# Kernel tuning notes

Hardware: AMD Instinct MI355X
Metric: run time of the kernel (lower is better)

## Reference

```python
import jax, jax.numpy as jnp
import numpy as np
from math import sqrt

MUL = 256        # multiplicity of every irrep slot
N = 20000        # batch (edges/nodes)
FS = MUL * 1 * MUL  # flat size of each uvw weight path (u=256, v=1, w=256)

def _cg_tensors():
    # real-basis Wigner-3j (Clebsch-Gordan) tensors for l <= 1, e3nn normalization (sum of squares = 1)
    C000 = np.ones((1, 1, 1))
    eye3 = np.eye(3) / sqrt(3.0)
    C011 = eye3.reshape(1, 3, 3)
    C101 = eye3.reshape(3, 1, 3)
    C110 = eye3.reshape(3, 3, 1)
    eps = np.zeros((3, 3, 3))
    eps[0, 1, 2] = eps[1, 2, 0] = eps[2, 0, 1] = 1.0
    eps[0, 2, 1] = eps[2, 1, 0] = eps[1, 0, 2] = -1.0
    C111 = eps / sqrt(6.0)
    return C000, C011, C101, C110, C111

_C000, _C011, _C101, _C110, _C111 = [jnp.asarray(c, dtype=jnp.float32) for c in _cg_tensors()]

# normalization: alpha = sqrt((2*l_out+1) / sum_{paths with same i_out} mul1*mul2)
_A0 = sqrt(1.0 / (2 * MUL))   # l_out=0: dim 1, fan sum = 256+256 = 512
_A1 = sqrt(3.0 / (3 * MUL))   # l_out=1: dim 3, fan sum = 256*3 = 768

# (i_in1, i_in2, i_out, CG, alpha) — order defines weight layout
PATHS = [
    (0, 0, 0, _C000, _A0),
    (0, 1, 1, _C011, _A1),
    (1, 0, 1, _C101, _A1),
    (1, 1, 0, _C110, _A0),
    (1, 1, 1, _C111, _A1),
]

def setup_inputs() -> dict:
    key = jax.random.key(0)
    k1, k2, k3 = jax.random.split(key, 3)
    x1 = jax.random.normal(k1, (N, 4 * MUL), dtype=jnp.float32)   # 256x0e (256) + 256x1e (768)
    x2 = jax.random.normal(k2, (N, 4), dtype=jnp.float32)         # 1x0e (1) + 1x1e (3)
    w = jax.random.normal(k3, (5 * FS,), dtype=jnp.float32)
    # rescale=True: scale init weights by 1/sqrt(slices_fan_in[i_out]); fan_in(uvw)=mul1*mul2=256
    k0 = 1.0 / sqrt(2 * MUL)   # i_out=0: 256+256
    k1_ = 1.0 / sqrt(3 * MUL)  # i_out=1: 256*3
    scales = jnp.concatenate([jnp.full((FS,), s, dtype=jnp.float32) for s in (k0, k1_, k1_, k0, k1_)])
    weight = w * scales
    return {"x1": x1, "x2": x2, "weight": weight}

def reference(x1, x2, weight):
    n = x1.shape[0]
    x1_segs = (x1[:, :MUL].reshape(n, MUL, 1), x1[:, MUL:].reshape(n, MUL, 3))
    x2_segs = (x2[:, :1].reshape(n, 1, 1), x2[:, 1:].reshape(n, 1, 3))
    outs = [jnp.zeros((n, MUL, 1), x1.dtype), jnp.zeros((n, MUL, 3), x1.dtype)]
    off = 0
    for (ia, ib, io, cg, alpha) in PATHS:
        w = weight[off:off + FS].reshape(MUL, 1, MUL)
        off += FS
        outs[io] = outs[io] + alpha * jnp.einsum('uvw,ijk,zui,zvj->zwk', w, cg, x1_segs[ia], x2_segs[ib])
    return jnp.concatenate([outs[0].reshape(n, MUL), outs[1].reshape(n, 3 * MUL)], axis=-1)
```

## Files before the change

kernel.cpp:

```cpp
#include <hip/hip_runtime.h>


typedef short bf16x8 __attribute__((ext_vector_type(8)));
typedef float f32x4 __attribute__((ext_vector_type(4)));
typedef int   ni4   __attribute__((ext_vector_type(4)));

static __device__ __forceinline__ unsigned short f2bf(float f) {
  unsigned int u = __builtin_bit_cast(unsigned int, f);
  u += 0x7FFFu + ((u >> 16) & 1u);
  return (unsigned short)(u >> 16);
}

static __device__ __forceinline__ bf16x8 asbf(int4 v) {
  return __builtin_bit_cast(bf16x8, v);
}
static __device__ __forceinline__ bf16x8 asbfn(ni4 v) {
  return __builtin_bit_cast(bf16x8, v);
}

static __device__ __forceinline__ void gload4(ni4& dst, const void* p) {
  asm volatile("global_load_dwordx4 %0, %1, off" : "=v"(dst) : "v"(p));
}

#define WAITV(n) do { \
    asm volatile("s_waitcnt vmcnt(" #n ")"); \
    __builtin_amdgcn_sched_barrier(0); \
  } while (0)

__global__ __launch_bounds__(256) void prep_weights(
    const float* __restrict__ wgt, unsigned short* __restrict__ Bw)
{
  int fid = blockIdx.x * 256 + threadIdx.x;
  union { unsigned short h[8]; int4 v; } pk;
  if (fid < 24576) {
    int lane = fid & 63;
    int ct = (fid >> 6) & 15;
    int q = fid >> 10;
    int kt = q % 3, c = q / 3;
    int w = ct * 16 + (lane & 15);
    int kh = (lane >> 4) * 8;
#pragma unroll
    for (int e = 0; e < 8; ++e) {
      int kc = kt * 32 + kh + e;
      int seg = kc >> 5;
      int u = c * 32 + (kc & 31);
      float s  = (seg == 2) ? 0.025515518153991442f : 0.03608439182435161f;
      int off  = (seg == 0) ? 65536 : (seg == 1 ? 131072 : 262144);
      pk.h[e] = f2bf(wgt[off + u * 256 + w] * s);
    }
    ((int4*)Bw)[fid] = pk.v;
  } else if (fid < 40960) {
    int f2 = fid - 24576;
    int lane = f2 & 63;
    int ct = (f2 >> 6) & 15;
    int q = f2 >> 10;
    int kt = q & 1, c = q >> 1;
    int w = ct * 16 + (lane & 15);
    int kh = (lane >> 4) * 8;
#pragma unroll
    for (int e = 0; e < 8; ++e) {
      int kc = kt * 32 + kh + e;
      int seg = kc >> 5;
      int u = c * 32 + (kc & 31);
      float s  = (seg == 0) ? 0.04419417382415922f : 0.025515518153991442f;
      int off  = (seg == 0) ? 0 : 196608;
      pk.h[e] = f2bf(wgt[off + u * 256 + w] * s);
    }
    ((int4*)Bw)[fid] = pk.v;
  }
}

#define WSLOTS 704
#define T0BASE 576

struct X1Raw { ni4 a[8]; };

static __device__ __forceinline__ void load_x1_asm(
    X1Raw& r, const float* __restrict__ x1, int zrow, int ub, int rr)
{
  const float* base = x1 + (size_t)zrow * 1024;
  const float* ps = base + ub + rr * 8;
  gload4(r.a[0], ps);
  gload4(r.a[1], ps + 4);
  const float* pv = base + 256 + 3 * ub + rr * 24;
#pragma unroll
  for (int i = 0; i < 6; ++i) gload4(r.a[2 + i], pv + 4 * i);
}

static __device__ __forceinline__ void build_frags(
    const X1Raw& r, int zl, int rr, float s2, const float* v2, int4* wbuf)
{
  union { float4 q[2]; float f[8]; } s1u;
  s1u.q[0] = __builtin_bit_cast(float4, r.a[0]);
  s1u.q[1] = __builtin_bit_cast(float4, r.a[1]);
  union { float4 q[6]; float f[24]; } v1u;
#pragma unroll
  for (int i = 0; i < 6; ++i) v1u.q[i] = __builtin_bit_cast(float4, r.a[2 + i]);

#pragma unroll
  for (int sg = 0; sg < 3; ++sg) {
#pragma unroll
    for (int k = 0; k < 3; ++k) {
      int row = 3 * zl + k;
      int fl  = (((rr << 4) | (row & 15)) ^ sg) ^ rr;
      int slot = (row >> 4) * 192 + sg * 64 + fl;
      float t[8];
      if (sg == 0) {
#pragma unroll
        for (int e = 0; e < 8; ++e) t[e] = s1u.f[e] * v2[k];
      } else if (sg == 1) {
#pragma unroll
        for (int e = 0; e < 8; ++e) t[e] = v1u.f[3 * e + k] * s2;
      } else {
        int k1 = k + 1; if (k1 > 2) k1 -= 3;
        int k2 = k + 2; if (k2 > 2) k2 -= 3;
#pragma unroll
        for (int e = 0; e < 8; ++e)
          t[e] = v1u.f[3 * e + k1] * v2[k2] - v1u.f[3 * e + k2] * v2[k1];
      }
      union { unsigned short h[8]; int4 v; } pk;
#pragma unroll
      for (int e = 0; e < 8; ++e) pk.h[e] = f2bf(t[e]);
      wbuf[slot] = pk.v;
    }
  }
#pragma unroll
  for (int sg = 0; sg < 2; ++sg) {
    int fl = (((rr << 4) | zl) ^ sg) ^ rr;
    int slot = T0BASE + sg * 64 + fl;
    float t[8];
    if (sg == 0) {
#pragma unroll
      for (int e = 0; e < 8; ++e) t[e] = s1u.f[e] * s2;
    } else {
#pragma unroll
      for (int e = 0; e < 8; ++e) {
        const float* p = v1u.f + 3 * e;
        t[e] = p[0] * v2[0] + p[1] * v2[1] + p[2] * v2[2];
      }
    }
    union { unsigned short h[8]; int4 v; } pk;
#pragma unroll
    for (int e = 0; e < 8; ++e) pk.h[e] = f2bf(t[e]);
    wbuf[slot] = pk.v;
  }
}

static __device__ __forceinline__ void burstB(
    ni4 (&vb)[20], const int4* __restrict__ B1v,
    const int4* __restrict__ B0v, int c, int ct0, int lane)
{
#pragma unroll
  for (int kt = 0; kt < 3; ++kt)
#pragma unroll
    for (int j = 0; j < 4; ++j)
      gload4(vb[kt * 4 + j],
             B1v + ((size_t)((c * 3 + kt) * 16 + ct0 + j)) * 64 + lane);
#pragma unroll
  for (int kt = 0; kt < 2; ++kt)
#pragma unroll
    for (int j = 0; j < 4; ++j)
      gload4(vb[12 + kt * 4 + j],
             B0v + ((size_t)((c * 2 + kt) * 16 + ct0 + j)) * 64 + lane);
}

static __device__ __forceinline__ void gemm_steps(
    const int4* __restrict__ wbuf, const ni4 (&vb)[20], int lane,
    f32x4 acc1[3][4], f32x4 acc0[4])
{
  __builtin_amdgcn_s_setprio(1);
#pragma unroll
  for (int kt = 0; kt < 3; ++kt) {
    int fl = (lane ^ kt) ^ (lane >> 4);
    int4 a[3];
#pragma unroll
    for (int rt = 0; rt < 3; ++rt) a[rt] = wbuf[rt * 192 + kt * 64 + fl];
#pragma unroll
    for (int rt = 0; rt < 3; ++rt) {
      bf16x8 av = asbf(a[rt]);
#pragma unroll
      for (int j = 0; j < 4; ++j)
        acc1[rt][j] = __builtin_amdgcn_mfma_f32_16x16x32_bf16(
            av, asbfn(vb[kt * 4 + j]), acc1[rt][j], 0, 0, 0);
    }
  }
#pragma unroll
  for (int kt = 0; kt < 2; ++kt) {
    int fl = (lane ^ kt) ^ (lane >> 4);
    int4 a0 = wbuf[T0BASE + kt * 64 + fl];
    bf16x8 av = asbf(a0);
#pragma unroll
    for (int j = 0; j < 4; ++j)
      acc0[j] = __builtin_amdgcn_mfma_f32_16x16x32_bf16(
          av, asbfn(vb[12 + kt * 4 + j]), acc0[j], 0, 0, 0);
  }
  __builtin_amdgcn_s_setprio(0);
}

__global__ __launch_bounds__(256, 2) void tp_main(
    const float* __restrict__ x1, const float* __restrict__ x2,
    const int4* __restrict__ B1v, const int4* __restrict__ B0v,
    float* __restrict__ out)
{
  __shared__ int4 ldsT[4 * WSLOTS];
  const int tid  = threadIdx.x;
  const int lane = tid & 63;
  const int wid  = tid >> 6;
  const int ct0  = wid * 4;
  const int z0   = blockIdx.x * 16;
  const int zl   = lane >> 2;
  const int rr   = lane & 3;
  int4* wbuf = ldsT + wid * WSLOTS;

  f32x4 acc1[3][4];
  f32x4 acc0[4];
#pragma unroll
  for (int i = 0; i < 3; ++i)
#pragma unroll
    for (int j = 0; j < 4; ++j) acc1[i][j] = (f32x4){0.f, 0.f, 0.f, 0.f};
#pragma unroll
  for (int j = 0; j < 4; ++j) acc0[j] = (f32x4){0.f, 0.f, 0.f, 0.f};

  ni4 x2raw;
  gload4(x2raw, x2 + (size_t)(z0 + zl) * 4);
  WAITV(0);
  float4 x2v = __builtin_bit_cast(float4, x2raw);
  const float s2 = x2v.x;
  float v2[3] = {x2v.y, x2v.z, x2v.w};

  X1Raw rX;
  ni4 vb[20];

  load_x1_asm(rX, x1, z0 + zl, 0, rr);

#pragma unroll 1
  for (int c = 0; c < 7; ++c) {
    burstB(vb, B1v, B0v, c, ct0, lane);
    WAITV(20);
    build_frags(rX, zl, rr, s2, v2, wbuf);
    load_x1_asm(rX, x1, z0 + zl, (c + 1) * 32, rr);
    WAITV(8);
    gemm_steps(wbuf, vb, lane, acc1, acc0);
  }
  burstB(vb, B1v, B0v, 7, ct0, lane);
  WAITV(20);
  build_frags(rX, zl, rr, s2, v2, wbuf);
  WAITV(0);
  gemm_steps(wbuf, vb, lane, acc1, acc0);

  const int col = lane & 15;
  const int rb  = (lane >> 4) * 4;
#pragma unroll
  for (int j = 0; j < 4; ++j) {
    int w = (ct0 + j) * 16 + col;
#pragma unroll
    for (int rg = 0; rg < 4; ++rg) {
      int row = rb + rg;
      out[(size_t)(z0 + row) * 1024 + w] = acc0[j][rg];
    }
  }
#pragma unroll
  for (int rt = 0; rt < 3; ++rt) {
#pragma unroll
    for (int j = 0; j < 4; ++j) {
      int w = (ct0 + j) * 16 + col;
#pragma unroll
      for (int rg = 0; rg < 4; ++rg) {
        int row = rt * 16 + rb + rg;
        int zz = row / 3;
        int k  = row - zz * 3;
        out[(size_t)(z0 + zz) * 1024 + 256 + w * 3 + k] = acc1[rt][j][rg];
      }
    }
  }
}

extern "C" void kernel_launch(void* const* d_in, const int* in_sizes, int n_in,
                              void* d_out, int out_size, void* d_ws, size_t ws_size,
                              hipStream_t stream) {
  const float* x1  = (const float*)d_in[0];
  const float* x2  = (const float*)d_in[1];
  const float* wgt = (const float*)d_in[2];
  float* out = (float*)d_out;

  unsigned short* Bw = (unsigned short*)d_ws;
  const int4* B1v = (const int4*)Bw;
  const int4* B0v = B1v + 24576;

  int n = in_sizes[0] / 1024;

  prep_weights<<<160, 256, 0, stream>>>(wgt, Bw);
  tp_main<<<n / 16, 256, 0, stream>>>(x1, x2, B1v, B0v, out);
}
```

Baseline: 77.29 us.

## Split work into single-wave blocks over column quarters and use packed bf16 convert

Restructures tp_main so each block is one wave computing 32 output columns for 16 rows, with eight blocks per row tile instead of four waves sharing a block. This shrinks accumulator and B-register footprint and raises block count and occupancy. In exchange, the x1 outer-product fragment construction and x1 loads are duplicated across twice as many waves. Replaces the software float-to-bf16 rounding with the hardware v_cvt_pk_bf16_f32 packed convert to cut VALU work.

```diff
diff --git a/kernel.cpp b/kernel.cpp
--- a/kernel.cpp
+++ b/kernel.cpp
@@ -9,6 +9,12 @@
   unsigned int u = __builtin_bit_cast(unsigned int, f);
   u += 0x7FFFu + ((u >> 16) & 1u);
   return (unsigned short)(u >> 16);
+}
+
+static __device__ __forceinline__ int cvtpk(float lo, float hi) {
+  int r;
+  asm("v_cvt_pk_bf16_f32 %0, %1, %2" : "=v"(r) : "v"(lo), "v"(hi));
+  return r;
 }
 
 static __device__ __forceinline__ bf16x8 asbf(int4 v) {
@@ -70,7 +76,6 @@
   }
 }
 
-#define WSLOTS 704
 #define T0BASE 576
 
 struct X1Raw { ni4 a[8]; };
@@ -118,10 +123,10 @@
         for (int e = 0; e < 8; ++e)
           t[e] = v1u.f[3 * e + k1] * v2[k2] - v1u.f[3 * e + k2] * v2[k1];
       }
-      union { unsigned short h[8]; int4 v; } pk;
-#pragma unroll
-      for (int e = 0; e < 8; ++e) pk.h[e] = f2bf(t[e]);
-      wbuf[slot] = pk.v;
+      int4 pk;
+      pk.x = cvtpk(t[0], t[1]); pk.y = cvtpk(t[2], t[3]);
+      pk.z = cvtpk(t[4], t[5]); pk.w = cvtpk(t[6], t[7]);
+      wbuf[slot] = pk;
     }
   }
 #pragma unroll
@@ -139,34 +144,34 @@
         t[e] = p[0] * v2[0] + p[1] * v2[1] + p[2] * v2[2];
       }
     }
-    union { unsigned short h[8]; int4 v; } pk;
-#pragma unroll
-    for (int e = 0; e < 8; ++e) pk.h[e] = f2bf(t[e]);
-    wbuf[slot] = pk.v;
+    int4 pk;
+    pk.x = cvtpk(t[0], t[1]); pk.y = cvtpk(t[2], t[3]);
+    pk.z = cvtpk(t[4], t[5]); pk.w = cvtpk(t[6], t[7]);
+    wbuf[slot] = pk;
   }
 }
 
 static __device__ __forceinline__ void burstB(
-    ni4 (&vb)[20], const int4* __restrict__ B1v,
+    ni4 (&vb)[10], const int4* __restrict__ B1v,
     const int4* __restrict__ B0v, int c, int ct0, int lane)
 {
 #pragma unroll
   for (int kt = 0; kt < 3; ++kt)
 #pragma unroll
-    for (int j = 0; j < 4; ++j)
-      gload4(vb[kt * 4 + j],
+    for (int j = 0; j < 2; ++j)
+      gload4(vb[kt * 2 + j],
              B1v + ((size_t)((c * 3 + kt) * 16 + ct0 + j)) * 64 + lane);
 #pragma unroll
   for (int kt = 0; kt < 2; ++kt)
 #pragma unroll
-    for (int j = 0; j < 4; ++j)
-      gload4(vb[12 + kt * 4 + j],
+    for (int j = 0; j < 2; ++j)
+      gload4(vb[6 + kt * 2 + j],
              B0v + ((size_t)((c * 2 + kt) * 16 + ct0 + j)) * 64 + lane);
 }
 
 static __device__ __forceinline__ void gemm_steps(
-    const int4* __restrict__ wbuf, const ni4 (&vb)[20], int lane,
-    f32x4 acc1[3][4], f32x4 acc0[4])
+    const int4* __restrict__ wbuf, const ni4 (&vb)[10], int lane,
+    f32x4 acc1[3][2], f32x4 acc0[2])
 {
   __builtin_amdgcn_s_setprio(1);
 #pragma unroll
@@ -179,9 +184,9 @@
     for (int rt = 0; rt < 3; ++rt) {
       bf16x8 av = asbf(a[rt]);
 #pragma unroll
-      for (int j = 0; j < 4; ++j)
+      for (int j = 0; j < 2; ++j)
         acc1[rt][j] = __builtin_amdgcn_mfma_f32_16x16x32_bf16(
-            av, asbfn(vb[kt * 4 + j]), acc1[rt][j], 0, 0, 0);
+            av, asbfn(vb[kt * 2 + j]), acc1[rt][j], 0, 0, 0);
     }
   }
 #pragma unroll
@@ -190,36 +195,34 @@
     int4 a0 = wbuf[T0BASE + kt * 64 + fl];
     bf16x8 av = asbf(a0);
 #pragma unroll
-    for (int j = 0; j < 4; ++j)
+    for (int j = 0; j < 2; ++j)
       acc0[j] = __builtin_amdgcn_mfma_f32_16x16x32_bf16(
-          av, asbfn(vb[12 + kt * 4 + j]), acc0[j], 0, 0, 0);
+          av, asbfn(vb[6 + kt * 2 + j]), acc0[j], 0, 0, 0);
   }
   __builtin_amdgcn_s_setprio(0);
 }
 
-__global__ __launch_bounds__(256, 2) void tp_main(
+__global__ __launch_bounds__(64, 3) void tp_main(
     const float* __restrict__ x1, const float* __restrict__ x2,
     const int4* __restrict__ B1v, const int4* __restrict__ B0v,
     float* __restrict__ out)
 {
-  __shared__ int4 ldsT[4 * WSLOTS];
-  const int tid  = threadIdx.x;
-  const int lane = tid & 63;
-  const int wid  = tid >> 6;
-  const int ct0  = wid * 4;
-  const int z0   = blockIdx.x * 16;
+  __shared__ int4 wbuf[704];
+  const int lane = threadIdx.x & 63;
+  const int colq = blockIdx.x & 7;
+  const int ct0  = colq * 2;
+  const int z0   = (blockIdx.x >> 3) * 16;
   const int zl   = lane >> 2;
   const int rr   = lane & 3;
-  int4* wbuf = ldsT + wid * WSLOTS;
-
-  f32x4 acc1[3][4];
-  f32x4 acc0[4];
+
+  f32x4 acc1[3][2];
+  f32x4 acc0[2];
 #pragma unroll
   for (int i = 0; i < 3; ++i)
 #pragma unroll
-    for (int j = 0; j < 4; ++j) acc1[i][j] = (f32x4){0.f, 0.f, 0.f, 0.f};
-#pragma unroll
-  for (int j = 0; j < 4; ++j) acc0[j] = (f32x4){0.f, 0.f, 0.f, 0.f};
+    for (int j = 0; j < 2; ++j) acc1[i][j] = (f32x4){0.f, 0.f, 0.f, 0.f};
+#pragma unroll
+  for (int j = 0; j < 2; ++j) acc0[j] = (f32x4){0.f, 0.f, 0.f, 0.f};
 
   ni4 x2raw;
   gload4(x2raw, x2 + (size_t)(z0 + zl) * 4);
@@ -229,21 +232,21 @@
   float v2[3] = {x2v.y, x2v.z, x2v.w};
 
   X1Raw rX;
-  ni4 vb[20];
+  ni4 vb[10];
 
   load_x1_asm(rX, x1, z0 + zl, 0, rr);
 
 #pragma unroll 1
   for (int c = 0; c < 7; ++c) {
     burstB(vb, B1v, B0v, c, ct0, lane);
-    WAITV(20);
+    WAITV(10);
     build_frags(rX, zl, rr, s2, v2, wbuf);
     load_x1_asm(rX, x1, z0 + zl, (c + 1) * 32, rr);
     WAITV(8);
     gemm_steps(wbuf, vb, lane, acc1, acc0);
   }
   burstB(vb, B1v, B0v, 7, ct0, lane);
-  WAITV(20);
+  WAITV(10);
   build_frags(rX, zl, rr, s2, v2, wbuf);
   WAITV(0);
   gemm_steps(wbuf, vb, lane, acc1, acc0);
@@ -251,7 +254,7 @@
   const int col = lane & 15;
   const int rb  = (lane >> 4) * 4;
 #pragma unroll
-  for (int j = 0; j < 4; ++j) {
+  for (int j = 0; j < 2; ++j) {
     int w = (ct0 + j) * 16 + col;
 #pragma unroll
     for (int rg = 0; rg < 4; ++rg) {
@@ -262,7 +265,7 @@
 #pragma unroll
   for (int rt = 0; rt < 3; ++rt) {
 #pragma unroll
-    for (int j = 0; j < 4; ++j) {
+    for (int j = 0; j < 2; ++j) {
       int w = (ct0 + j) * 16 + col;
 #pragma unroll
       for (int rg = 0; rg < 4; ++rg) {
@@ -290,5 +293,5 @@
   int n = in_sizes[0] / 1024;
 
   prep_weights<<<160, 256, 0, stream>>>(wgt, Bw);
-  tp_main<<<n / 16, 256, 0, stream>>>(x1, x2, B1v, B0v, out);
-}
+  tp_main<<<(n / 16) * 8, 64, 0, stream>>>(x1, x2, B1v, B0v, out);
+}
```

Measured after the change: 117.8 us. +52.4%, slower.
